# Optimization experiments

Hardware: AMD Instinct MI355X
Metric: run time of the kernel (lower is better)

## Reference

```python
import jax, jax.numpy as jnp
import numpy as np

N_NODES = 100000
N_EDGES = 1600000
D_IN = 128
D_H = 128
N_CLASSES = 64


def setup_inputs() -> dict:
    key = jax.random.key(0)
    ks = jax.random.split(key, 8)
    feat = jax.random.normal(ks[0], (N_NODES, D_IN), dtype=jnp.float32)
    src = jax.random.randint(ks[1], (N_EDGES,), 0, N_NODES)
    dst = jax.random.randint(ks[2], (N_EDGES,), 0, N_NODES)
    # Xavier-ish scaled weights (nn.Linear layout: [out, in])
    W1 = jax.random.normal(ks[3], (D_H, D_IN), dtype=jnp.float32) * (1.0 / np.sqrt(D_IN))
    b1 = jnp.zeros((D_H,), dtype=jnp.float32)
    W2 = jax.random.normal(ks[4], (D_H, D_H), dtype=jnp.float32) * (1.0 / np.sqrt(D_H))
    b2 = jnp.zeros((D_H,), dtype=jnp.float32)
    Wl = jax.random.normal(ks[5], (N_CLASSES, 2 * D_H), dtype=jnp.float32) * (1.0 / np.sqrt(2 * D_H))
    bl = jnp.zeros((N_CLASSES,), dtype=jnp.float32)
    return {"feat": feat, "src": src, "dst": dst, "W1": W1, "b1": b1,
            "W2": W2, "b2": b2, "Wl": Wl, "bl": bl}


def _mean_agg(h, src, dst, inv_deg, n):
    # copy_u('h','m') + mean('m','neigh'): gather src features, segment-sum on dst, divide by in-degree
    s = jax.ops.segment_sum(h[src], dst, num_segments=n)  # [N, D]
    return s * inv_deg


def reference(feat, src, dst, W1, b1, W2, b2, Wl, bl):
    n = feat.shape[0]
    deg = jax.ops.segment_sum(jnp.ones_like(dst, dtype=feat.dtype), dst, num_segments=n)
    inv_deg = (1.0 / jnp.maximum(deg, 1.0))[:, None]  # zero-degree nodes -> 0 (sum is 0 anyway)
    h1 = jax.nn.relu(_mean_agg(feat, src, dst, inv_deg, n) @ W1.T + b1)
    h2 = jax.nn.relu(_mean_agg(h1, src, dst, inv_deg, n) @ W2.T + b2)
    logits = jnp.concatenate([h1, h2], axis=-1) @ Wl.T + bl
    return jax.nn.log_softmax(logits, axis=-1)
```

## Files before the change

kernel.cpp:

```cpp
#include <hip/hip_runtime.h>
#include <stdint.h>

#define D 128
#define NCLS 64
#define BSH 7
#define NBMAX 1024
#define CCHUNK 4096

typedef __bf16 bf16x8 __attribute__((ext_vector_type(8)));
typedef float f32x4 __attribute__((ext_vector_type(4)));

union B8 { uint4 u; bf16x8 v; };


__global__ __launch_bounds__(256) void k_prep(const float* __restrict__ feat,
                                              const float* __restrict__ W1,
                                              const float* __restrict__ W2,
                                              const float* __restrict__ Wl,
                                              ushort* __restrict__ featb,
                                              ushort* __restrict__ W1b,
                                              ushort* __restrict__ W2b,
                                              ushort* __restrict__ Wlb, int n8feat) {
  const int n1 = D * D / 8;
  const int nl = 2 * D * NCLS / 8;
  int t = blockIdx.x * 256 + threadIdx.x;
  const float* xp; ushort* yp; int idx;
  if (t < n8feat) { xp = feat; yp = featb; idx = t; }
  else {
    t -= n8feat;
    if (t < n1) { xp = W1; yp = W1b; idx = t; }
    else if (t < 2 * n1) { xp = W2; yp = W2b; idx = t - n1; }
    else if (t < 2 * n1 + nl) { xp = Wl; yp = Wlb; idx = t - 2 * n1; }
    else return;
  }
  const float4 a = reinterpret_cast<const float4*>(xp)[idx * 2 + 0];
  const float4 b = reinterpret_cast<const float4*>(xp)[idx * 2 + 1];
  union { __bf16 h[8]; uint4 u; } p;
  p.h[0] = (__bf16)a.x; p.h[1] = (__bf16)a.y; p.h[2] = (__bf16)a.z; p.h[3] = (__bf16)a.w;
  p.h[4] = (__bf16)b.x; p.h[5] = (__bf16)b.y; p.h[6] = (__bf16)b.z; p.h[7] = (__bf16)b.w;
  reinterpret_cast<uint4*>(yp)[idx] = p.u;
}


__global__ __launch_bounds__(256) void k_bhist(const int* __restrict__ dst,
                                               int* __restrict__ bcnt, int E, int NB) {
  __shared__ int h[NBMAX];
  for (int i = threadIdx.x; i < NB; i += 256) h[i] = 0;
  __syncthreads();
  for (int e = blockIdx.x * 256 + threadIdx.x; e < E; e += gridDim.x * 256)
    atomicAdd(&h[dst[e] >> BSH], 1);
  __syncthreads();
  for (int i = threadIdx.x; i < NB; i += 256) {
    int c = h[i];
    if (c) atomicAdd(&bcnt[i], c);
  }
}

__global__ __launch_bounds__(1024) void k_bscan(const int* __restrict__ bcnt,
                                                int* __restrict__ bbase,
                                                int* __restrict__ bcur, int NB, int E) {
  __shared__ int sm[NBMAX];
  const int tid = threadIdx.x;
  int v = (tid < NB) ? bcnt[tid] : 0;
  sm[tid] = v;
  __syncthreads();
  for (int off = 1; off < NBMAX; off <<= 1) {
    int t = (tid >= off) ? sm[tid - off] : 0;
    __syncthreads();
    sm[tid] += t;
    __syncthreads();
  }
  if (tid < NB) {
    bbase[tid] = sm[tid] - v;
    bcur[tid] = sm[tid] - v;
  }
  if (tid == 0) bbase[NB] = E;
}

__global__ __launch_bounds__(256) void k_bscatter(const int* __restrict__ src,
                                                  const int* __restrict__ dst,
                                                  int* __restrict__ bcur,
                                                  int* __restrict__ ebuck, int E, int NB) {
  __shared__ int h[NBMAX];
  __shared__ int base[NBMAX];
  const int beg = blockIdx.x * CCHUNK;
  const int end = min(beg + CCHUNK, E);
  for (int i = threadIdx.x; i < NB; i += 256) h[i] = 0;
  __syncthreads();
  for (int e = beg + threadIdx.x; e < end; e += 256)
    atomicAdd(&h[dst[e] >> BSH], 1);
  __syncthreads();
  for (int i = threadIdx.x; i < NB; i += 256) {
    int c = h[i];
    base[i] = c ? atomicAdd(&bcur[i], c) : 0;
    h[i] = 0;
  }
  __syncthreads();
  for (int e = beg + threadIdx.x; e < end; e += 256) {
    const int d = dst[e];
    const int b = d >> BSH;
    const int r = atomicAdd(&h[b], 1);
    ebuck[base[b] + r] = (src[e] << BSH) | (d & 127);
  }
}

__global__ __launch_bounds__(256) void k_bbuild(const int* __restrict__ ebuck,
                                                const int* __restrict__ bbase,
                                                int* __restrict__ row_ptr,
                                                int* __restrict__ esrc,
                                                float* __restrict__ inv, int N, int E) {
  __shared__ int cnt[128], s[128], cur[128];
  const int b = blockIdx.x;
  const int n0 = b << BSH;
  const int nn = min(128, N - n0);
  const int beg = bbase[b], end = bbase[b + 1];
  const int tid = threadIdx.x;
  if (tid < 128) cnt[tid] = 0;
  __syncthreads();
  for (int e = beg + tid; e < end; e += 256)
    atomicAdd(&cnt[ebuck[e] & 127], 1);
  __syncthreads();
  if (tid < 128) s[tid] = cnt[tid];
  __syncthreads();
  for (int off = 1; off < 128; off <<= 1) {
    int t = (tid < 128 && tid >= off) ? s[tid - off] : 0;
    __syncthreads();
    if (tid < 128) s[tid] += t;
    __syncthreads();
  }
  if (tid < 128) {
    const int ex = s[tid] - cnt[tid];
    cur[tid] = ex;
    if (tid < nn) {
      row_ptr[n0 + tid] = beg + ex;
      inv[n0 + tid] = 1.0f / fmaxf((float)cnt[tid], 1.0f);
    }
  }
  if (b == 0 && tid == 0) row_ptr[N] = E;
  __syncthreads();
  for (int e = beg + tid; e < end; e += 256) {
    const int p = ebuck[e];
    const int r = atomicAdd(&cur[p & 127], 1);
    esrc[beg + r] = p >> BSH;
  }
}


__global__ __launch_bounds__(256) void k_gather_mean(const ushort* __restrict__ h,
                                                     const int* __restrict__ row_ptr,
                                                     const int* __restrict__ esrc,
                                                     const float* __restrict__ inv,
                                                     ushort* __restrict__ out, int N) {
  const int node = blockIdx.x * 4 + (threadIdx.x >> 6);
  if (node >= N) return;
  const int lane = threadIdx.x & 63;
  const int beg = row_ptr[node];
  const int end = row_ptr[node + 1];
  const ushort* hp = h + lane * 2;
  float ax = 0.f, ay = 0.f, bx = 0.f, by = 0.f;
  int e = beg;
  for (; e + 7 < end; e += 8) {
    const int s0 = esrc[e + 0];
    const int s1 = esrc[e + 1];
    const int s2 = esrc[e + 2];
    const int s3 = esrc[e + 3];
    const int s4 = esrc[e + 4];
    const int s5 = esrc[e + 5];
    const int s6 = esrc[e + 6];
    const int s7 = esrc[e + 7];
    const unsigned int u0 = *reinterpret_cast<const unsigned int*>(hp + (size_t)s0 * D);
    const unsigned int u1 = *reinterpret_cast<const unsigned int*>(hp + (size_t)s1 * D);
    const unsigned int u2 = *reinterpret_cast<const unsigned int*>(hp + (size_t)s2 * D);
    const unsigned int u3 = *reinterpret_cast<const unsigned int*>(hp + (size_t)s3 * D);
    const unsigned int u4 = *reinterpret_cast<const unsigned int*>(hp + (size_t)s4 * D);
    const unsigned int u5 = *reinterpret_cast<const unsigned int*>(hp + (size_t)s5 * D);
    const unsigned int u6 = *reinterpret_cast<const unsigned int*>(hp + (size_t)s6 * D);
    const unsigned int u7 = *reinterpret_cast<const unsigned int*>(hp + (size_t)s7 * D);
    ax += __uint_as_float(u0 << 16) + __uint_as_float(u1 << 16);
    ay += __uint_as_float(u0 & 0xffff0000u) + __uint_as_float(u1 & 0xffff0000u);
    bx += __uint_as_float(u2 << 16) + __uint_as_float(u3 << 16);
    by += __uint_as_float(u2 & 0xffff0000u) + __uint_as_float(u3 & 0xffff0000u);
    ax += __uint_as_float(u4 << 16) + __uint_as_float(u5 << 16);
    ay += __uint_as_float(u4 & 0xffff0000u) + __uint_as_float(u5 & 0xffff0000u);
    bx += __uint_as_float(u6 << 16) + __uint_as_float(u7 << 16);
    by += __uint_as_float(u6 & 0xffff0000u) + __uint_as_float(u7 & 0xffff0000u);
  }
  if (e + 3 < end) {
    const int s0 = esrc[e + 0];
    const int s1 = esrc[e + 1];
    const int s2 = esrc[e + 2];
    const int s3 = esrc[e + 3];
    const unsigned int u0 = *reinterpret_cast<const unsigned int*>(hp + (size_t)s0 * D);
    const unsigned int u1 = *reinterpret_cast<const unsigned int*>(hp + (size_t)s1 * D);
    const unsigned int u2 = *reinterpret_cast<const unsigned int*>(hp + (size_t)s2 * D);
    const unsigned int u3 = *reinterpret_cast<const unsigned int*>(hp + (size_t)s3 * D);
    ax += __uint_as_float(u0 << 16) + __uint_as_float(u1 << 16);
    ay += __uint_as_float(u0 & 0xffff0000u) + __uint_as_float(u1 & 0xffff0000u);
    bx += __uint_as_float(u2 << 16) + __uint_as_float(u3 << 16);
    by += __uint_as_float(u2 & 0xffff0000u) + __uint_as_float(u3 & 0xffff0000u);
    e += 4;
  }
  if (e + 1 < end) {
    const int s0 = esrc[e + 0];
    const int s1 = esrc[e + 1];
    const unsigned int u0 = *reinterpret_cast<const unsigned int*>(hp + (size_t)s0 * D);
    const unsigned int u1 = *reinterpret_cast<const unsigned int*>(hp + (size_t)s1 * D);
    ax += __uint_as_float(u0 << 16) + __uint_as_float(u1 << 16);
    ay += __uint_as_float(u0 & 0xffff0000u) + __uint_as_float(u1 & 0xffff0000u);
    e += 2;
  }
  if (e < end) {
    const unsigned int u0 = *reinterpret_cast<const unsigned int*>(hp + (size_t)esrc[e] * D);
    ax += __uint_as_float(u0 << 16);
    ay += __uint_as_float(u0 & 0xffff0000u);
  }
  ax += bx;
  ay += by;
  const float iv = inv[node];
  union { __bf16 b[2]; unsigned int u; } p;
  p.b[0] = (__bf16)(ax * iv);
  p.b[1] = (__bf16)(ay * iv);
  *reinterpret_cast<unsigned int*>(out + (size_t)node * D + lane * 2) = p.u;
}


__global__ __launch_bounds__(256) void k_gemm_mfma(const ushort* __restrict__ A,
                                                   const ushort* __restrict__ Wb,
                                                   const float* __restrict__ bias,
                                                   ushort* __restrict__ Hout, int N) {
  const int wave = threadIdx.x >> 6;
  const int lane = threadIdx.x & 63;
  const int l15 = lane & 15;
  const int quad = lane >> 4;

  B8 bfrag[2][4];
  float bv[2];
#pragma unroll
  for (int t = 0; t < 2; ++t) {
    const int n = wave * 32 + t * 16 + l15;
    bv[t] = bias[n];
#pragma unroll
    for (int ks = 0; ks < 4; ++ks)
      bfrag[t][ks].u = *reinterpret_cast<const uint4*>(Wb + n * D + ks * 32 + quad * 8);
  }

  const int mtiles = N >> 4;
  for (int mt = blockIdx.x; mt < mtiles; mt += gridDim.x) {
    const ushort* ap = A + (size_t)(mt * 16 + l15) * D + quad * 8;
    B8 a0, a1, a2, a3;
    a0.u = *reinterpret_cast<const uint4*>(ap);
    a1.u = *reinterpret_cast<const uint4*>(ap + 32);
    a2.u = *reinterpret_cast<const uint4*>(ap + 64);
    a3.u = *reinterpret_cast<const uint4*>(ap + 96);
#pragma unroll
    for (int t = 0; t < 2; ++t) {
      f32x4 acc = {0.f, 0.f, 0.f, 0.f};
      acc = __builtin_amdgcn_mfma_f32_16x16x32_bf16(a0.v, bfrag[t][0].v, acc, 0, 0, 0);
      acc = __builtin_amdgcn_mfma_f32_16x16x32_bf16(a1.v, bfrag[t][1].v, acc, 0, 0, 0);
      acc = __builtin_amdgcn_mfma_f32_16x16x32_bf16(a2.v, bfrag[t][2].v, acc, 0, 0, 0);
      acc = __builtin_amdgcn_mfma_f32_16x16x32_bf16(a3.v, bfrag[t][3].v, acc, 0, 0, 0);
      const int col = wave * 32 + t * 16 + l15;
#pragma unroll
      for (int r = 0; r < 4; ++r) {
        const int row = mt * 16 + quad * 4 + r;
        const float v = fmaxf(acc[r] + bv[t], 0.f);
        union { __bf16 b; ushort s; } c;
        c.b = (__bf16)v;
        Hout[(size_t)row * D + col] = c.s;
      }
    }
  }
}


__global__ __launch_bounds__(256) void k_gemm2_logits(const ushort* __restrict__ A2,
                                                      const ushort* __restrict__ H1,
                                                      const ushort* __restrict__ W2b,
                                                      const float* __restrict__ b2,
                                                      const ushort* __restrict__ Wlb,
                                                      const float* __restrict__ bl,
                                                      float* __restrict__ out, int N) {
  __shared__ ushort H2t[16][136];
  __shared__ float L[16][NCLS + 4];
  const int wave = threadIdx.x >> 6;
  const int lane = threadIdx.x & 63;
  const int l15 = lane & 15;
  const int quad = lane >> 4;

  B8 bfrag2[2][4];
  float bv2[2];
#pragma unroll
  for (int t = 0; t < 2; ++t) {
    const int n = wave * 32 + t * 16 + l15;
    bv2[t] = b2[n];
#pragma unroll
    for (int ks = 0; ks < 4; ++ks)
      bfrag2[t][ks].u = *reinterpret_cast<const uint4*>(W2b + n * D + ks * 32 + quad * 8);
  }
  B8 bfragL[8];
  const int nl = wave * 16 + l15;
  const float bbl = bl[nl];
#pragma unroll
  for (int ks = 0; ks < 8; ++ks)
    bfragL[ks].u = *reinterpret_cast<const uint4*>(Wlb + nl * (2 * D) + ks * 32 + quad * 8);

  const int mtiles = N >> 4;
  for (int mt = blockIdx.x; mt < mtiles; mt += gridDim.x) {
    const ushort* ap = A2 + (size_t)(mt * 16 + l15) * D + quad * 8;
    B8 a0, a1, a2, a3;
    a0.u = *reinterpret_cast<const uint4*>(ap);
    a1.u = *reinterpret_cast<const uint4*>(ap + 32);
    a2.u = *reinterpret_cast<const uint4*>(ap + 64);
    a3.u = *reinterpret_cast<const uint4*>(ap + 96);
#pragma unroll
    for (int t = 0; t < 2; ++t) {
      f32x4 acc = {0.f, 0.f, 0.f, 0.f};
      acc = __builtin_amdgcn_mfma_f32_16x16x32_bf16(a0.v, bfrag2[t][0].v, acc, 0, 0, 0);
      acc = __builtin_amdgcn_mfma_f32_16x16x32_bf16(a1.v, bfrag2[t][1].v, acc, 0, 0, 0);
      acc = __builtin_amdgcn_mfma_f32_16x16x32_bf16(a2.v, bfrag2[t][2].v, acc, 0, 0, 0);
      acc = __builtin_amdgcn_mfma_f32_16x16x32_bf16(a3.v, bfrag2[t][3].v, acc, 0, 0, 0);
      const int col = wave * 32 + t * 16 + l15;
#pragma unroll
      for (int r = 0; r < 4; ++r) {
        const float v = fmaxf(acc[r] + bv2[t], 0.f);
        union { __bf16 b; ushort s; } c;
        c.b = (__bf16)v;
        H2t[quad * 4 + r][col] = c.s;
      }
    }
    __syncthreads();
    const size_t rb = (size_t)(mt * 16 + l15) * D + quad * 8;
    f32x4 acc = {0.f, 0.f, 0.f, 0.f};
    B8 a;
#pragma unroll
    for (int ks = 0; ks < 4; ++ks) {
      a.u = *reinterpret_cast<const uint4*>(H1 + rb + ks * 32);
      acc = __builtin_amdgcn_mfma_f32_16x16x32_bf16(a.v, bfragL[ks].v, acc, 0, 0, 0);
    }
#pragma unroll
    for (int ks = 0; ks < 4; ++ks) {
      a.u = *reinterpret_cast<const uint4*>(&H2t[l15][ks * 32 + quad * 8]);
      acc = __builtin_amdgcn_mfma_f32_16x16x32_bf16(a.v, bfragL[4 + ks].v, acc, 0, 0, 0);
    }
#pragma unroll
    for (int r = 0; r < 4; ++r)
      L[quad * 4 + r][wave * 16 + l15] = acc[r] + bbl;
    __syncthreads();
#pragma unroll
    for (int r = 0; r < 4; ++r) {
      const int row = wave * 4 + r;
      float v = L[row][lane];
      float m = v;
#pragma unroll
      for (int off = 32; off > 0; off >>= 1) m = fmaxf(m, __shfl_xor(m, off));
      float e = __expf(v - m);
#pragma unroll
      for (int off = 32; off > 0; off >>= 1) e += __shfl_xor(e, off);
      out[(size_t)(mt * 16 + row) * NCLS + lane] = v - m - __logf(e);
    }
    __syncthreads();
  }
}


extern "C" void kernel_launch(void* const* d_in, const int* in_sizes, int n_in,
                              void* d_out, int out_size, void* d_ws, size_t ws_size,
                              hipStream_t stream) {
  const float* feat = (const float*)d_in[0];
  const int* src = (const int*)d_in[1];
  const int* dst = (const int*)d_in[2];
  const float* W1 = (const float*)d_in[3];
  const float* b1 = (const float*)d_in[4];
  const float* W2 = (const float*)d_in[5];
  const float* b2 = (const float*)d_in[6];
  const float* Wl = (const float*)d_in[7];
  const float* bl = (const float*)d_in[8];
  float* out = (float*)d_out;

  const int N = in_sizes[0] / D;
  const int E = in_sizes[1];
  const int NB = (N + 127) >> BSH;

  float* ws = (float*)d_ws;
  float* inv = ws;
  ushort* featb = (ushort*)(inv + N);
  ushort* scratch = featb + (size_t)N * D;
  ushort* h1b = scratch + (size_t)N * D;
  int* row_ptr = (int*)(h1b + (size_t)N * D);
  int* esrc = row_ptr + N + 1;
  int* bcnt = esrc + E;
  int* bbase = bcnt + NBMAX;
  int* bcur = bbase + NBMAX + 1;
  ushort* W1b = (ushort*)(bcur + NBMAX);
  ushort* W2b = W1b + D * D;
  ushort* Wlb = W2b + D * D;
  int* ebuck = (int*)scratch;

  hipMemsetAsync(bcnt, 0, NBMAX * sizeof(int), stream);

  const int n8 = N * D / 8;
  const int prepTot = n8 + 2 * (D * D / 8) + (2 * D * NCLS / 8);
  k_prep<<<(prepTot + 255) / 256, 256, 0, stream>>>(feat, W1, W2, Wl,
                                                    featb, W1b, W2b, Wlb, n8);

  k_bhist<<<256, 256, 0, stream>>>(dst, bcnt, E, NB);
  k_bscan<<<1, 1024, 0, stream>>>(bcnt, bbase, bcur, NB, E);
  k_bscatter<<<(E + CCHUNK - 1) / CCHUNK, 256, 0, stream>>>(src, dst, bcur, ebuck, E, NB);
  k_bbuild<<<NB, 256, 0, stream>>>(ebuck, bbase, row_ptr, esrc, inv, N, E);

  const int gatherBlocks = (N + 3) / 4;
  ushort* aggb = scratch;

  k_gather_mean<<<gatherBlocks, 256, 0, stream>>>(featb, row_ptr, esrc, inv, aggb, N);
  k_gemm_mfma<<<2048, 256, 0, stream>>>(aggb, W1b, b1, h1b, N);

  k_gather_mean<<<gatherBlocks, 256, 0, stream>>>(h1b, row_ptr, esrc, inv, aggb, N);
  k_gemm2_logits<<<2048, 256, 0, stream>>>(aggb, h1b, W2b, b2, Wlb, bl, out, N);
}
```

Before: 372.7 us.

## Gather with 16-byte loads across 4 edge lanes, fold memset into prep

```diff
diff --git a/kernel.cpp b/kernel.cpp
--- a/kernel.cpp
+++ b/kernel.cpp
@@ -20,10 +20,12 @@
                                               ushort* __restrict__ featb,
                                               ushort* __restrict__ W1b,
                                               ushort* __restrict__ W2b,
-                                              ushort* __restrict__ Wlb, int n8feat) {
+                                              ushort* __restrict__ Wlb,
+                                              int* __restrict__ bcnt, int n8feat) {
   const int n1 = D * D / 8;
   const int nl = 2 * D * NCLS / 8;
   int t = blockIdx.x * 256 + threadIdx.x;
+  if (t < NBMAX) bcnt[t] = 0;
   const float* xp; ushort* yp; int idx;
   if (t < n8feat) { xp = feat; yp = featb; idx = t; }
   else {
@@ -146,6 +148,17 @@
 }
 
 
+__device__ __forceinline__ void acc8(float* acc, const uint4& u) {
+  acc[0] += __uint_as_float(u.x << 16);
+  acc[1] += __uint_as_float(u.x & 0xffff0000u);
+  acc[2] += __uint_as_float(u.y << 16);
+  acc[3] += __uint_as_float(u.y & 0xffff0000u);
+  acc[4] += __uint_as_float(u.z << 16);
+  acc[5] += __uint_as_float(u.z & 0xffff0000u);
+  acc[6] += __uint_as_float(u.w << 16);
+  acc[7] += __uint_as_float(u.w & 0xffff0000u);
+}
+
 __global__ __launch_bounds__(256) void k_gather_mean(const ushort* __restrict__ h,
                                                      const int* __restrict__ row_ptr,
                                                      const int* __restrict__ esrc,
@@ -154,75 +167,90 @@
   const int node = blockIdx.x * 4 + (threadIdx.x >> 6);
   if (node >= N) return;
   const int lane = threadIdx.x & 63;
+  const int q = lane >> 4;
+  const int w = lane & 15;
   const int beg = row_ptr[node];
   const int end = row_ptr[node + 1];
-  const ushort* hp = h + lane * 2;
-  float ax = 0.f, ay = 0.f, bx = 0.f, by = 0.f;
+  const ushort* hp = h + w * 8;
+  float acc[8] = {0.f, 0.f, 0.f, 0.f, 0.f, 0.f, 0.f, 0.f};
   int e = beg;
-  for (; e + 7 < end; e += 8) {
-    const int s0 = esrc[e + 0];
-    const int s1 = esrc[e + 1];
-    const int s2 = esrc[e + 2];
-    const int s3 = esrc[e + 3];
-    const int s4 = esrc[e + 4];
-    const int s5 = esrc[e + 5];
-    const int s6 = esrc[e + 6];
-    const int s7 = esrc[e + 7];
-    const unsigned int u0 = *reinterpret_cast<const unsigned int*>(hp + (size_t)s0 * D);
-    const unsigned int u1 = *reinterpret_cast<const unsigned int*>(hp + (size_t)s1 * D);
-    const unsigned int u2 = *reinterpret_cast<const unsigned int*>(hp + (size_t)s2 * D);
-    const unsigned int u3 = *reinterpret_cast<const unsigned int*>(hp + (size_t)s3 * D);
-    const unsigned int u4 = *reinterpret_cast<const unsigned int*>(hp + (size_t)s4 * D);
-    const unsigned int u5 = *reinterpret_cast<const unsigned int*>(hp + (size_t)s5 * D);
-    const unsigned int u6 = *reinterpret_cast<const unsigned int*>(hp + (size_t)s6 * D);
-    const unsigned int u7 = *reinterpret_cast<const unsigned int*>(hp + (size_t)s7 * D);
-    ax += __uint_as_float(u0 << 16) + __uint_as_float(u1 << 16);
-    ay += __uint_as_float(u0 & 0xffff0000u) + __uint_as_float(u1 & 0xffff0000u);
-    bx += __uint_as_float(u2 << 16) + __uint_as_float(u3 << 16);
-    by += __uint_as_float(u2 & 0xffff0000u) + __uint_as_float(u3 & 0xffff0000u);
-    ax += __uint_as_float(u4 << 16) + __uint_as_float(u5 << 16);
-    ay += __uint_as_float(u4 & 0xffff0000u) + __uint_as_float(u5 & 0xffff0000u);
-    bx += __uint_as_float(u6 << 16) + __uint_as_float(u7 << 16);
-    by += __uint_as_float(u6 & 0xffff0000u) + __uint_as_float(u7 & 0xffff0000u);
+  for (; e + 15 < end; e += 16) {
+    const int s0 = esrc[e + q];
+    const int s1 = esrc[e + 4 + q];
+    const int s2 = esrc[e + 8 + q];
+    const int s3 = esrc[e + 12 + q];
+    const uint4 u0 = *reinterpret_cast<const uint4*>(hp + (size_t)s0 * D);
+    const uint4 u1 = *reinterpret_cast<const uint4*>(hp + (size_t)s1 * D);
+    const uint4 u2 = *reinterpret_cast<const uint4*>(hp + (size_t)s2 * D);
+    const uint4 u3 = *reinterpret_cast<const uint4*>(hp + (size_t)s3 * D);
+    acc8(acc, u0);
+    acc8(acc, u1);
+    acc8(acc, u2);
+    acc8(acc, u3);
+  }
+  if (e + 7 < end) {
+    const int s0 = esrc[e + q];
+    const int s1 = esrc[e + 4 + q];
+    const uint4 u0 = *reinterpret_cast<const uint4*>(hp + (size_t)s0 * D);
+    const uint4 u1 = *reinterpret_cast<const uint4*>(hp + (size_t)s1 * D);
+    acc8(acc, u0);
+    acc8(acc, u1);
+    e += 8;
   }
   if (e + 3 < end) {
-    const int s0 = esrc[e + 0];
-    const int s1 = esrc[e + 1];
-    const int s2 = esrc[e + 2];
-    const int s3 = esrc[e + 3];
-    const unsigned int u0 = *reinterpret_cast<const unsigned int*>(hp + (size_t)s0 * D);
-    const unsigned int u1 = *reinterpret_cast<const unsigned int*>(hp + (size_t)s1 * D);
-    const unsigned int u2 = *reinterpret_cast<const unsigned int*>(hp + (size_t)s2 * D);
-    const unsigned int u3 = *reinterpret_cast<const unsigned int*>(hp + (size_t)s3 * D);
-    ax += __uint_as_float(u0 << 16) + __uint_as_float(u1 << 16);
-    ay += __uint_as_float(u0 & 0xffff0000u) + __uint_as_float(u1 & 0xffff0000u);
-    bx += __uint_as_float(u2 << 16) + __uint_as_float(u3 << 16);
-    by += __uint_as_float(u2 & 0xffff0000u) + __uint_as_float(u3 & 0xffff0000u);
+    const int s0 = esrc[e + q];
+    const uint4 u0 = *reinterpret_cast<const uint4*>(hp + (size_t)s0 * D);
+    acc8(acc, u0);
     e += 4;
   }
-  if (e + 1 < end) {
-    const int s0 = esrc[e + 0];
-    const int s1 = esrc[e + 1];
-    const unsigned int u0 = *reinterpret_cast<const unsigned int*>(hp + (size_t)s0 * D);
-    const unsigned int u1 = *reinterpret_cast<const unsigned int*>(hp + (size_t)s1 * D);
-    ax += __uint_as_float(u0 << 16) + __uint_as_float(u1 << 16);
-    ay += __uint_as_float(u0 & 0xffff0000u) + __uint_as_float(u1 & 0xffff0000u);
-    e += 2;
-  }
-  if (e < end) {
-    const unsigned int u0 = *reinterpret_cast<const unsigned int*>(hp + (size_t)esrc[e] * D);
-    ax += __uint_as_float(u0 << 16);
-    ay += __uint_as_float(u0 & 0xffff0000u);
-  }
-  ax += bx;
-  ay += by;
-  const float iv = inv[node];
-  union { __bf16 b[2]; unsigned int u; } p;
-  p.b[0] = (__bf16)(ax * iv);
-  p.b[1] = (__bf16)(ay * iv);
-  *reinterpret_cast<unsigned int*>(out + (size_t)node * D + lane * 2) = p.u;
-}
-
+  if (e + q < end) {
+    const int s0 = esrc[e + q];
+    const uint4 u0 = *reinterpret_cast<const uint4*>(hp + (size_t)s0 * D);
+    acc8(acc, u0);
+  }
+#pragma unroll
+  for (int i = 0; i < 8; ++i) {
+    acc[i] += __shfl_xor(acc[i], 16);
+    acc[i] += __shfl_xor(acc[i], 32);
+  }
+  if (q == 0) {
+    const float iv = inv[node];
+    union { __bf16 b[8]; uint4 u; } p;
+#pragma unroll
+    for (int i = 0; i < 8; ++i) p.b[i] = (__bf16)(acc[i] * iv);
+    *reinterpret_cast<uint4*>(out + (size_t)node * D + w * 8) = p.u;
+  }
+}
+
+
+__device__ __forceinline__ void gemm_tile16(const ushort* __restrict__ A,
+                                            const B8 bfrag[2][4], const float bv[2],
+                                            ushort* __restrict__ Hout, int mt,
+                                            int l15, int quad, int wave) {
+  const ushort* ap = A + (size_t)(mt * 16 + l15) * D + quad * 8;
+  B8 a0, a1, a2, a3;
+  a0.u = *reinterpret_cast<const uint4*>(ap);
+  a1.u = *reinterpret_cast<const uint4*>(ap + 32);
+  a2.u = *reinterpret_cast<const uint4*>(ap + 64);
+  a3.u = *reinterpret_cast<const uint4*>(ap + 96);
+#pragma unroll
+  for (int t = 0; t < 2; ++t) {
+    f32x4 acc = {0.f, 0.f, 0.f, 0.f};
+    acc = __builtin_amdgcn_mfma_f32_16x16x32_bf16(a0.v, bfrag[t][0].v, acc, 0, 0, 0);
+    acc = __builtin_amdgcn_mfma_f32_16x16x32_bf16(a1.v, bfrag[t][1].v, acc, 0, 0, 0);
+    acc = __builtin_amdgcn_mfma_f32_16x16x32_bf16(a2.v, bfrag[t][2].v, acc, 0, 0, 0);
+    acc = __builtin_amdgcn_mfma_f32_16x16x32_bf16(a3.v, bfrag[t][3].v, acc, 0, 0, 0);
+    const int col = wave * 32 + t * 16 + l15;
+#pragma unroll
+    for (int r = 0; r < 4; ++r) {
+      const int row = mt * 16 + quad * 4 + r;
+      const float v = fmaxf(acc[r] + bv[t], 0.f);
+      union { __bf16 b; ushort s; } c;
+      c.b = (__bf16)v;
+      Hout[(size_t)row * D + col] = c.s;
+    }
+  }
+}
 
 __global__ __launch_bounds__(256) void k_gemm_mfma(const ushort* __restrict__ A,
                                                    const ushort* __restrict__ Wb,
@@ -245,31 +273,13 @@
   }
 
   const int mtiles = N >> 4;
-  for (int mt = blockIdx.x; mt < mtiles; mt += gridDim.x) {
-    const ushort* ap = A + (size_t)(mt * 16 + l15) * D + quad * 8;
-    B8 a0, a1, a2, a3;
-    a0.u = *reinterpret_cast<const uint4*>(ap);
-    a1.u = *reinterpret_cast<const uint4*>(ap + 32);
-    a2.u = *reinterpret_cast<const uint4*>(ap + 64);
-    a3.u = *reinterpret_cast<const uint4*>(ap + 96);
-#pragma unroll
-    for (int t = 0; t < 2; ++t) {
-      f32x4 acc = {0.f, 0.f, 0.f, 0.f};
-      acc = __builtin_amdgcn_mfma_f32_16x16x32_bf16(a0.v, bfrag[t][0].v, acc, 0, 0, 0);
-      acc = __builtin_amdgcn_mfma_f32_16x16x32_bf16(a1.v, bfrag[t][1].v, acc, 0, 0, 0);
-      acc = __builtin_amdgcn_mfma_f32_16x16x32_bf16(a2.v, bfrag[t][2].v, acc, 0, 0, 0);
-      acc = __builtin_amdgcn_mfma_f32_16x16x32_bf16(a3.v, bfrag[t][3].v, acc, 0, 0, 0);
-      const int col = wave * 32 + t * 16 + l15;
-#pragma unroll
-      for (int r = 0; r < 4; ++r) {
-        const int row = mt * 16 + quad * 4 + r;
-        const float v = fmaxf(acc[r] + bv[t], 0.f);
-        union { __bf16 b; ushort s; } c;
-        c.b = (__bf16)v;
-        Hout[(size_t)row * D + col] = c.s;
-      }
-    }
-  }
+  const int pairs = mtiles >> 1;
+  for (int p = blockIdx.x; p < pairs; p += gridDim.x) {
+    gemm_tile16(A, bfrag, bv, Hout, p * 2 + 0, l15, quad, wave);
+    gemm_tile16(A, bfrag, bv, Hout, p * 2 + 1, l15, quad, wave);
+  }
+  if ((mtiles & 1) && blockIdx.x == 0)
+    gemm_tile16(A, bfrag, bv, Hout, mtiles - 1, l15, quad, wave);
 }
 
 
@@ -396,12 +406,10 @@
   ushort* Wlb = W2b + D * D;
   int* ebuck = (int*)scratch;
 
-  hipMemsetAsync(bcnt, 0, NBMAX * sizeof(int), stream);
-
   const int n8 = N * D / 8;
   const int prepTot = n8 + 2 * (D * D / 8) + (2 * D * NCLS / 8);
   k_prep<<<(prepTot + 255) / 256, 256, 0, stream>>>(feat, W1, W2, Wl,
-                                                    featb, W1b, W2b, Wlb, n8);
+                                                    featb, W1b, W2b, Wlb, bcnt, n8);
 
   k_bhist<<<256, 256, 0, stream>>>(dst, bcnt, E, NB);
   k_bscan<<<1, 1024, 0, stream>>>(bcnt, bbase, bcur, NB, E);
```

After: 366.8 us. No clear change (-1.6%).
